# Kernel tuning notes

Hardware: AMD Instinct MI355X
Metric: run time of the kernel (lower is better)

The kernel has to match this reference:

```python
import jax, jax.numpy as jnp
import numpy as np

B, S, E, C, H = 64, 2048, 512, 512, 256


def setup_inputs() -> dict:
    key = jax.random.key(0)
    ks = jax.random.split(key, 8)
    encoder_word_embeds = jax.random.normal(ks[0], (B, S, E), dtype=jnp.float32)
    encoder_lengths = jax.random.randint(ks[1], (B,), 1, S + 1)  # lengths in [1, S]
    context_state = jax.random.normal(ks[2], (B, C), dtype=jnp.float32)
    # Learned parameters (nn.Linear style: y = x @ W.T + b)
    sw = 1.0 / np.sqrt(E)
    sc = 1.0 / np.sqrt(C)
    sh = 1.0 / np.sqrt(H)
    W_word = jax.random.uniform(ks[3], (H, E), minval=-sw, maxval=sw, dtype=jnp.float32)
    b_word = jax.random.uniform(ks[4], (H,), minval=-sw, maxval=sw, dtype=jnp.float32)
    W_ctx = jax.random.uniform(ks[5], (H, C), minval=-sc, maxval=sc, dtype=jnp.float32)
    b_ctx = jax.random.uniform(ks[6], (H,), minval=-sc, maxval=sc, dtype=jnp.float32)
    w_hidden = jax.random.uniform(ks[7], (H,), minval=-sh, maxval=sh, dtype=jnp.float32)  # hidden_layer has no bias
    return {
        "encoder_word_embeds": encoder_word_embeds,
        "encoder_lengths": encoder_lengths,
        "context_state": context_state,
        "W_word": W_word,
        "b_word": b_word,
        "W_ctx": W_ctx,
        "b_ctx": b_ctx,
        "w_hidden": w_hidden,
    }


def reference(encoder_word_embeds, encoder_lengths, context_state, W_word, b_word, W_ctx, b_ctx, w_hidden):
    seq_len = encoder_word_embeds.shape[1]
    # word mask [B, S]: positions < length
    positions = jnp.arange(seq_len)  # [S]
    mask = (positions[None, :] < encoder_lengths[:, None]).astype(jnp.float32)  # [B, S]
    # additive attention MLP
    word_feat = jnp.einsum("bse,he->bsh", encoder_word_embeds, W_word) + b_word  # [B,S,H]
    ctx_feat = context_state @ W_ctx.T + b_ctx  # [B,H]
    scores = jnp.einsum("bsh,h->bs", jnp.tanh(word_feat + ctx_feat[:, None, :]), w_hidden)  # [B,S]
    # softmax over seq, then mask and renormalize (matches original order)
    attn = jax.nn.softmax(scores, axis=1) * mask
    attn = attn / (1e-10 + attn.sum(axis=1, keepdims=True))  # [B,S]
    attention_features = jnp.einsum("bs,bse->be", attn, encoder_word_embeds)  # [B,E]
    return attention_features, attn
```

## Files before the change

### kernel.cpp

```cpp
#include <hip/hip_runtime.h>
#include <hip/hip_bf16.h>
#include <cstdint>
#include <cstddef>

#define B_  64
#define S_  2048
#define E_  512
#define C_  512
#define H_  256

using f32x4 = __attribute__((ext_vector_type(4))) float;
using s16x8 = __attribute__((ext_vector_type(8))) short;

__device__ __forceinline__ uint2 f4_to_bf4(float4 v) {
    __hip_bfloat162 lo = __float22bfloat162_rn(make_float2(v.x, v.y));
    __hip_bfloat162 hi = __float22bfloat162_rn(make_float2(v.z, v.w));
    union { __hip_bfloat162 b; unsigned u; } a, c;
    a.b = lo; c.b = hi;
    return make_uint2(a.u, c.u);
}

__device__ __forceinline__ void async16(const void* g, void* l) {
    __builtin_amdgcn_global_load_lds(
        (const __attribute__((address_space(1))) void*)g,
        (__attribute__((address_space(3))) void*)l,
        16, 0, 0);
}

__global__ void prep_kernel(const float* __restrict__ W, unsigned short* __restrict__ Wb,
                            const float* __restrict__ ctx, const float* __restrict__ Wc,
                            const float* __restrict__ bc, const float* __restrict__ bw,
                            float* __restrict__ cb) {
    __shared__ float row[C_];
    int blk = blockIdx.x, t = threadIdx.x;
    if (blk < 128) {
        int i = (blk * 256 + t) * 4;
        float4 v = *(const float4*)(W + i);
        *(uint2*)(Wb + i) = f4_to_bf4(v);
    } else {
        int b = blk - 128;
        row[t] = ctx[b * C_ + t];
        row[t + 256] = ctx[b * C_ + t + 256];
        __syncthreads();
        const float4* w4 = (const float4*)(Wc + (size_t)t * C_);
        const float4* x4 = (const float4*)row;
        float acc = 0.f;
        #pragma unroll 4
        for (int c = 0; c < C_ / 4; ++c) {
            float4 w = w4[c], x = x4[c];
            acc += w.x * x.x + w.y * x.y + w.z * x.z + w.w * x.w;
        }
        cb[b * H_ + t] = acc + bc[t] + bw[t];
    }
}

#define BM 128
#define BN 256
#define BK 64
#define LDT 72

__global__ __launch_bounds__(512) void scores_kernel(
    const float* __restrict__ A,
    const unsigned short* __restrict__ Wb,
    const float* __restrict__ cb,
    const float* __restrict__ wh,
    const int*   __restrict__ lens,
    float* __restrict__ scores)
{
    __shared__ __align__(16) unsigned short At[BM * LDT];
    __shared__ __align__(16) unsigned short Bt[BN * 64];
    __shared__ float sblk[BM];
    int t = threadIdx.x;
    int m0 = blockIdx.x * BM;
    int b  = m0 >> 11;
    int ms = m0 & (S_ - 1);
    if (ms >= lens[b]) return;

    int w = t >> 6, lane = t & 63, quad = lane >> 4, lm = lane & 15;
    int wm = (w & 1) * 64, wn = (w >> 1) * 64;

    if (t < BM) sblk[t] = 0.f;

    f32x4 acc[4][4] = {};

    int arow = t >> 4, acol = (t & 15) * 4;
    int la8 = lane >> 3, lc8 = lane & 7;

    for (int k0 = 0; k0 < E_; k0 += BK) {
        #pragma unroll
        for (int j = 0; j < 4; ++j) {
            int r  = (w << 5) + (j << 3) + la8;
            int cg = (lc8 ^ (r & 7)) << 3;
            async16(Wb + (size_t)r * E_ + k0 + cg,
                    (char*)Bt + (((w << 5) + (j << 3)) << 7));
        }
        #pragma unroll
        for (int i = 0; i < 4; ++i) {
            int r = arow + i * 32;
            float4 v = *(const float4*)(A + (size_t)(m0 + r) * E_ + k0 + acol);
            *(uint2*)(At + r * LDT + acol) = f4_to_bf4(v);
        }
        __syncthreads();
        #pragma unroll
        for (int ks = 0; ks < 2; ++ks) {
            s16x8 af[4], bfr[4];
            #pragma unroll
            for (int i = 0; i < 4; ++i)
                af[i] = *(const s16x8*)(At + (wm + i * 16 + lm) * LDT + ks * 32 + quad * 8);
            #pragma unroll
            for (int i = 0; i < 4; ++i) {
                int r = wn + i * 16 + lm;
                int c = (ks * 4 + quad) ^ (r & 7);
                bfr[i] = *(const s16x8*)(Bt + r * 64 + c * 8);
            }
            #pragma unroll
            for (int mi = 0; mi < 4; ++mi)
                #pragma unroll
                for (int ni = 0; ni < 4; ++ni)
                    acc[mi][ni] = __builtin_amdgcn_mfma_f32_16x16x32_bf16(
                        af[mi], bfr[ni], acc[mi][ni], 0, 0, 0);
        }
        __syncthreads();
    }

    float wv[4], cbv[4];
    #pragma unroll
    for (int ni = 0; ni < 4; ++ni) {
        int n = wn + ni * 16 + lm;
        wv[ni]  = wh[n];
        cbv[ni] = cb[b * H_ + n];
    }
    #pragma unroll
    for (int mi = 0; mi < 4; ++mi) {
        #pragma unroll
        for (int r = 0; r < 4; ++r) {
            float p = 0.f;
            #pragma unroll
            for (int ni = 0; ni < 4; ++ni) {
                float x = acc[mi][ni][r] + cbv[ni];
                x = fminf(fmaxf(x, -15.f), 15.f);
                float e = __expf(2.f * x);
                float th = 1.f - 2.f * __builtin_amdgcn_rcpf(e + 1.f);
                p += wv[ni] * th;
            }
            #pragma unroll
            for (int off = 8; off >= 1; off >>= 1)
                p += __shfl_xor(p, off);
            if (lm == 0)
                atomicAdd(&sblk[wm + mi * 16 + quad * 4 + r], p);
        }
    }
    __syncthreads();
    if (t < BM) scores[m0 + t] = sblk[t];
}

__global__ void softmax_kernel(const int* __restrict__ lens, float* __restrict__ attn,
                               float* __restrict__ feat) {
    __shared__ float redm[4], redt[4];
    int b = blockIdx.x, t = threadIdx.x;
    int len = lens[b];
    float* sc = attn + (size_t)b * S_;
    feat[b * E_ + t] = 0.f;
    feat[b * E_ + 256 + t] = 0.f;
    float v[8];
    #pragma unroll
    for (int i = 0; i < 8; ++i) {
        int s = t + i * 256;
        v[i] = (s < len) ? sc[s] : -1e30f;
    }
    float m = -1e30f;
    #pragma unroll
    for (int i = 0; i < 8; ++i) m = fmaxf(m, v[i]);
    #pragma unroll
    for (int off = 32; off >= 1; off >>= 1) m = fmaxf(m, __shfl_xor(m, off));
    if ((t & 63) == 0) redm[t >> 6] = m;
    __syncthreads();
    m = fmaxf(fmaxf(redm[0], redm[1]), fmaxf(redm[2], redm[3]));
    float e[8]; float tm = 0.f;
    #pragma unroll
    for (int i = 0; i < 8; ++i) {
        int s = t + i * 256;
        e[i] = (s < len) ? __expf(v[i] - m) : 0.f;
        tm += e[i];
    }
    #pragma unroll
    for (int off = 32; off >= 1; off >>= 1) tm += __shfl_xor(tm, off);
    if ((t & 63) == 0) redt[t >> 6] = tm;
    __syncthreads();
    tm = redt[0] + redt[1] + redt[2] + redt[3];
    float sfac = 1.f / tm;
    #pragma unroll
    for (int i = 0; i < 8; ++i) {
        int s = t + i * 256;
        sc[s] = e[i] * sfac;
    }
}

__global__ __launch_bounds__(512) void wsum_kernel(
    const float* __restrict__ A, const float* __restrict__ attn,
    const int* __restrict__ lens, float* __restrict__ out) {
    int b = blockIdx.y;
    int len = lens[b];
    int s0 = blockIdx.x * 128;
    if (s0 >= len) return;
    int send = s0 + 128; if (send > len) send = len;
    int t  = threadIdx.x;
    int e4 = t & 127;
    int sr = t >> 7;
    const float* ap = attn + (size_t)b * S_;
    f32x4 acc = {0.f, 0.f, 0.f, 0.f};
    const float* base = A + (size_t)b * S_ * E_;
    for (int s = s0 + sr; s < send; s += 4) {
        float wgt = ap[s];
        f32x4 v = *(const f32x4*)(base + (size_t)s * E_ + e4 * 4);
        acc += wgt * v;
    }
    __shared__ f32x4 red[4][128];
    red[sr][e4] = acc;
    __syncthreads();
    if (t < 128) {
        f32x4 tot = red[0][t] + red[1][t] + red[2][t] + red[3][t];
        float* o = out + (size_t)b * E_ + t * 4;
        atomicAdd(o + 0, tot[0]);
        atomicAdd(o + 1, tot[1]);
        atomicAdd(o + 2, tot[2]);
        atomicAdd(o + 3, tot[3]);
    }
}

extern "C" void kernel_launch(void* const* d_in, const int* in_sizes, int n_in,
                              void* d_out, int out_size, void* d_ws, size_t ws_size,
                              hipStream_t stream) {
    const float* embeds = (const float*)d_in[0];
    const int*   lens   = (const int*)d_in[1];
    const float* ctx    = (const float*)d_in[2];
    const float* Ww     = (const float*)d_in[3];
    const float* bw     = (const float*)d_in[4];
    const float* Wc     = (const float*)d_in[5];
    const float* bc     = (const float*)d_in[6];
    const float* wh     = (const float*)d_in[7];
    float* out  = (float*)d_out;
    float* feat = out;
    float* attn = out + B_ * E_;

    unsigned short* Wb = (unsigned short*)d_ws;
    float* cb = (float*)((char*)d_ws + (size_t)H_ * E_ * sizeof(unsigned short));

    prep_kernel<<<192, 256, 0, stream>>>(Ww, Wb, ctx, Wc, bc, bw, cb);
    scores_kernel<<<dim3(B_ * S_ / BM), 512, 0, stream>>>(embeds, Wb, cb, wh, lens, attn);
    softmax_kernel<<<B_, 256, 0, stream>>>(lens, attn, feat);
    wsum_kernel<<<dim3(S_ / 128, B_), 512, 0, stream>>>(embeds, attn, lens, feat);
}
```

Baseline: 407.4 us.

## Drop LDS staging in scores GEMM and load MFMA fragments directly from global

The scores kernel no longer stages A and W tiles in shared memory. Each wave now loads its bf16 W fragments and fp32 A rows straight from global memory into registers and converts A to bf16 in place. The block tile shrinks from 128 to 64 rows with 256 threads, and all four waves share the same A rows while splitting H. This removes the LDS traffic and the per-iteration barriers. In exchange, each A element is read from global (through the cache) by four waves, and the loads are uncoalesced 32-byte row segments with no software pipelining.

After: 522.4 us. +28.2%, slower.

```diff
diff --git a/kernel.cpp b/kernel.cpp
--- a/kernel.cpp
+++ b/kernel.cpp
@@ -20,11 +20,11 @@
     return make_uint2(a.u, c.u);
 }
 
-__device__ __forceinline__ void async16(const void* g, void* l) {
-    __builtin_amdgcn_global_load_lds(
-        (const __attribute__((address_space(1))) void*)g,
-        (__attribute__((address_space(3))) void*)l,
-        16, 0, 0);
+__device__ __forceinline__ s16x8 pack_bf8(float4 a, float4 b) {
+    union { s16x8 v; uint2 u[2]; } r;
+    r.u[0] = f4_to_bf4(a);
+    r.u[1] = f4_to_bf4(b);
+    return r.v;
 }
 
 __global__ void prep_kernel(const float* __restrict__ W, unsigned short* __restrict__ Wb,
@@ -54,12 +54,10 @@
     }
 }
 
-#define BM 128
-#define BN 256
+#define BM 64
 #define BK 64
-#define LDT 72
-
-__global__ __launch_bounds__(512) void scores_kernel(
+
+__global__ __launch_bounds__(256) void scores_kernel(
     const float* __restrict__ A,
     const unsigned short* __restrict__ Wb,
     const float* __restrict__ cb,
@@ -67,8 +65,6 @@
     const int*   __restrict__ lens,
     float* __restrict__ scores)
 {
-    __shared__ __align__(16) unsigned short At[BM * LDT];
-    __shared__ __align__(16) unsigned short Bt[BN * 64];
     __shared__ float sblk[BM];
     int t = threadIdx.x;
     int m0 = blockIdx.x * BM;
@@ -77,51 +73,43 @@
     if (ms >= lens[b]) return;
 
     int w = t >> 6, lane = t & 63, quad = lane >> 4, lm = lane & 15;
-    int wm = (w & 1) * 64, wn = (w >> 1) * 64;
+    int wn = w * 64;
 
     if (t < BM) sblk[t] = 0.f;
 
+    const float* a_base[4];
+    const unsigned short* b_base[4];
+    #pragma unroll
+    for (int i = 0; i < 4; ++i) {
+        a_base[i] = A  + (size_t)(m0 + i * 16 + lm) * E_ + quad * 8;
+        b_base[i] = Wb + (size_t)(wn + i * 16 + lm) * E_ + quad * 8;
+    }
+
     f32x4 acc[4][4] = {};
 
-    int arow = t >> 4, acol = (t & 15) * 4;
-    int la8 = lane >> 3, lc8 = lane & 7;
-
+    #pragma unroll 2
     for (int k0 = 0; k0 < E_; k0 += BK) {
         #pragma unroll
-        for (int j = 0; j < 4; ++j) {
-            int r  = (w << 5) + (j << 3) + la8;
-            int cg = (lc8 ^ (r & 7)) << 3;
-            async16(Wb + (size_t)r * E_ + k0 + cg,
-                    (char*)Bt + (((w << 5) + (j << 3)) << 7));
-        }
-        #pragma unroll
-        for (int i = 0; i < 4; ++i) {
-            int r = arow + i * 32;
-            float4 v = *(const float4*)(A + (size_t)(m0 + r) * E_ + k0 + acol);
-            *(uint2*)(At + r * LDT + acol) = f4_to_bf4(v);
-        }
-        __syncthreads();
-        #pragma unroll
         for (int ks = 0; ks < 2; ++ks) {
-            s16x8 af[4], bfr[4];
+            int ko = k0 + ks * 32;
+            s16x8 bfr[4];
             #pragma unroll
             for (int i = 0; i < 4; ++i)
-                af[i] = *(const s16x8*)(At + (wm + i * 16 + lm) * LDT + ks * 32 + quad * 8);
-            #pragma unroll
-            for (int i = 0; i < 4; ++i) {
-                int r = wn + i * 16 + lm;
-                int c = (ks * 4 + quad) ^ (r & 7);
-                bfr[i] = *(const s16x8*)(Bt + r * 64 + c * 8);
-            }
-            #pragma unroll
-            for (int mi = 0; mi < 4; ++mi)
+                bfr[i] = *(const s16x8*)(b_base[i] + ko);
+            #pragma unroll
+            for (int mi = 0; mi < 4; ++mi) {
+                const float* ap = a_base[mi] + ko;
+                float4 a0 = *(const float4*)ap;
+                float4 a1 = *(const float4*)(ap + 4);
+                s16x8 af = pack_bf8(a0, a1);
                 #pragma unroll
                 for (int ni = 0; ni < 4; ++ni)
                     acc[mi][ni] = __builtin_amdgcn_mfma_f32_16x16x32_bf16(
-                        af[mi], bfr[ni], acc[mi][ni], 0, 0, 0);
+                        af, bfr[ni], acc[mi][ni], 0, 0, 0);
+            }
         }
-        __syncthreads();
-    }
+    }
+    __syncthreads();
 
     float wv[4], cbv[4];
     #pragma unroll
@@ -147,7 +135,7 @@
             for (int off = 8; off >= 1; off >>= 1)
                 p += __shfl_xor(p, off);
             if (lm == 0)
-                atomicAdd(&sblk[wm + mi * 16 + quad * 4 + r], p);
+                atomicAdd(&sblk[mi * 16 + quad * 4 + r], p);
         }
     }
     __syncthreads();
@@ -247,7 +235,7 @@
     float* cb = (float*)((char*)d_ws + (size_t)H_ * E_ * sizeof(unsigned short));
 
     prep_kernel<<<192, 256, 0, stream>>>(Ww, Wb, ctx, Wc, bc, bw, cb);
-    scores_kernel<<<dim3(B_ * S_ / BM), 512, 0, stream>>>(embeds, Wb, cb, wh, lens, attn);
+    scores_kernel<<<dim3(B_ * S_ / BM), 256, 0, stream>>>(embeds, Wb, cb, wh, lens, attn);
     softmax_kernel<<<B_, 256, 0, stream>>>(lens, attn, feat);
     wsum_kernel<<<dim3(S_ / 128, B_), 512, 0, stream>>>(embeds, attn, lens, feat);
 }
```

## Fuse softmax and weighted sum into scores kernel via flash-style partials

Applied to the files above, without the earlier changes.

The scores kernel now computes a per-tile local max, exp-sum and exp-weighted sum of the embedding rows right after the scores, writing partial results to workspace. A small finalize kernel merges the partials with online-softmax rescaling, writes the features and normalizes the attention row. This removes the separate softmax and weighted-sum kernels and their second full read of the embeddings, which may now hit cache because the same tile was just loaded. In exchange the scores kernel gets a serial per-thread loop over 128 rows with strided fp32 loads, and the finalize step loops over partials serially.

Measured after the change: 418.9 us. +2.8%, slower.

```diff
diff --git a/kernel.cpp b/kernel.cpp
--- a/kernel.cpp
+++ b/kernel.cpp
@@ -65,16 +65,20 @@
     const float* __restrict__ cb,
     const float* __restrict__ wh,
     const int*   __restrict__ lens,
-    float* __restrict__ scores)
+    float* __restrict__ scores,
+    float* __restrict__ Wpart,
+    float* __restrict__ mtpart)
 {
     __shared__ __align__(16) unsigned short At[BM * LDT];
     __shared__ __align__(16) unsigned short Bt[BN * 64];
     __shared__ float sblk[BM];
+    __shared__ float pblk[BM];
     int t = threadIdx.x;
     int m0 = blockIdx.x * BM;
     int b  = m0 >> 11;
     int ms = m0 & (S_ - 1);
-    if (ms >= lens[b]) return;
+    int len = lens[b];
+    if (ms >= len) return;
 
     int w = t >> 6, lane = t & 63, quad = lane >> 4, lm = lane & 15;
     int wm = (w & 1) * 64, wn = (w >> 1) * 64;
@@ -152,79 +156,57 @@
     }
     __syncthreads();
     if (t < BM) scores[m0 + t] = sblk[t];
-}
-
-__global__ void softmax_kernel(const int* __restrict__ lens, float* __restrict__ attn,
-                               float* __restrict__ feat) {
-    __shared__ float redm[4], redt[4];
+
+    int nvalid = len - ms; if (nvalid > BM) nvalid = BM;
+    float m_l = -1e30f;
+    #pragma unroll 16
+    for (int r = 0; r < BM; ++r) {
+        float sv = (r < nvalid) ? sblk[r] : -1e30f;
+        m_l = fmaxf(m_l, sv);
+    }
+    if (t < BM) pblk[t] = (t < nvalid) ? __expf(sblk[t] - m_l) : 0.f;
+    __syncthreads();
+    float t_l = 0.f;
+    #pragma unroll 16
+    for (int r = 0; r < BM; ++r) t_l += pblk[r];
+    float accw = 0.f;
+    const float* ab = A + (size_t)m0 * E_ + t;
+    #pragma unroll 8
+    for (int r = 0; r < BM; ++r)
+        accw += pblk[r] * ab[(size_t)r * E_];
+    Wpart[(size_t)blockIdx.x * E_ + t] = accw;
+    if (t == 0) {
+        mtpart[blockIdx.x * 2 + 0] = m_l;
+        mtpart[blockIdx.x * 2 + 1] = t_l;
+    }
+}
+
+__global__ __launch_bounds__(512) void finalize_kernel(
+    const int* __restrict__ lens, const float* __restrict__ Wpart,
+    const float* __restrict__ mtpart,
+    float* __restrict__ attn,
+    float* __restrict__ feat)
+{
     int b = blockIdx.x, t = threadIdx.x;
     int len = lens[b];
+    int L = (len + BM - 1) / BM;
+    int base = b * (S_ / BM);
+    float M = -1e30f;
+    for (int l = 0; l < L; ++l) M = fmaxf(M, mtpart[(base + l) * 2]);
+    float T = 0.f;
+    for (int l = 0; l < L; ++l)
+        T += __expf(mtpart[(base + l) * 2] - M) * mtpart[(base + l) * 2 + 1];
+    float inv = 1.f / T;
+    float acc = 0.f;
+    for (int l = 0; l < L; ++l)
+        acc += __expf(mtpart[(base + l) * 2] - M) * Wpart[(size_t)(base + l) * E_ + t];
+    feat[b * E_ + t] = acc * inv;
     float* sc = attn + (size_t)b * S_;
-    feat[b * E_ + t] = 0.f;
-    feat[b * E_ + 256 + t] = 0.f;
-    float v[8];
     #pragma unroll
-    for (int i = 0; i < 8; ++i) {
-        int s = t + i * 256;
-        v[i] = (s < len) ? sc[s] : -1e30f;
-    }
-    float m = -1e30f;
-    #pragma unroll
-    for (int i = 0; i < 8; ++i) m = fmaxf(m, v[i]);
-    #pragma unroll
-    for (int off = 32; off >= 1; off >>= 1) m = fmaxf(m, __shfl_xor(m, off));
-    if ((t & 63) == 0) redm[t >> 6] = m;
-    __syncthreads();
-    m = fmaxf(fmaxf(redm[0], redm[1]), fmaxf(redm[2], redm[3]));
-    float e[8]; float tm = 0.f;
-    #pragma unroll
-    for (int i = 0; i < 8; ++i) {
-        int s = t + i * 256;
-        e[i] = (s < len) ? __expf(v[i] - m) : 0.f;
-        tm += e[i];
-    }
-    #pragma unroll
-    for (int off = 32; off >= 1; off >>= 1) tm += __shfl_xor(tm, off);
-    if ((t & 63) == 0) redt[t >> 6] = tm;
-    __syncthreads();
-    tm = redt[0] + redt[1] + redt[2] + redt[3];
-    float sfac = 1.f / tm;
-    #pragma unroll
-    for (int i = 0; i < 8; ++i) {
-        int s = t + i * 256;
-        sc[s] = e[i] * sfac;
-    }
-}
-
-__global__ __launch_bounds__(512) void wsum_kernel(
-    const float* __restrict__ A, const float* __restrict__ attn,
-    const int* __restrict__ lens, float* __restrict__ out) {
-    int b = blockIdx.y;
-    int len = lens[b];
-    int s0 = blockIdx.x * 128;
-    if (s0 >= len) return;
-    int send = s0 + 128; if (send > len) send = len;
-    int t  = threadIdx.x;
-    int e4 = t & 127;
-    int sr = t >> 7;
-    const float* ap = attn + (size_t)b * S_;
-    f32x4 acc = {0.f, 0.f, 0.f, 0.f};
-    const float* base = A + (size_t)b * S_ * E_;
-    for (int s = s0 + sr; s < send; s += 4) {
-        float wgt = ap[s];
-        f32x4 v = *(const f32x4*)(base + (size_t)s * E_ + e4 * 4);
-        acc += wgt * v;
-    }
-    __shared__ f32x4 red[4][128];
-    red[sr][e4] = acc;
-    __syncthreads();
-    if (t < 128) {
-        f32x4 tot = red[0][t] + red[1][t] + red[2][t] + red[3][t];
-        float* o = out + (size_t)b * E_ + t * 4;
-        atomicAdd(o + 0, tot[0]);
-        atomicAdd(o + 1, tot[1]);
-        atomicAdd(o + 2, tot[2]);
-        atomicAdd(o + 3, tot[3]);
+    for (int i = 0; i < 4; ++i) {
+        int s = t + i * 512;
+        float v = sc[s];
+        sc[s] = (s < len) ? __expf(v - M) * inv : 0.f;
     }
 }
 
@@ -243,11 +225,14 @@
     float* feat = out;
     float* attn = out + B_ * E_;
 
-    unsigned short* Wb = (unsigned short*)d_ws;
-    float* cb = (float*)((char*)d_ws + (size_t)H_ * E_ * sizeof(unsigned short));
+    char* ws = (char*)d_ws;
+    unsigned short* Wb = (unsigned short*)ws;
+    float* cb     = (float*)(ws + 256 * 1024);
+    float* Wpart  = (float*)(ws + 320 * 1024);
+    float* mtpart = (float*)(ws + 320 * 1024 + 2 * 1024 * 1024);
 
     prep_kernel<<<192, 256, 0, stream>>>(Ww, Wb, ctx, Wc, bc, bw, cb);
-    scores_kernel<<<dim3(B_ * S_ / BM), 512, 0, stream>>>(embeds, Wb, cb, wh, lens, attn);
-    softmax_kernel<<<B_, 256, 0, stream>>>(lens, attn, feat);
-    wsum_kernel<<<dim3(S_ / 128, B_), 512, 0, stream>>>(embeds, attn, lens, feat);
-}
+    scores_kernel<<<dim3(B_ * S_ / BM), 512, 0, stream>>>(embeds, Wb, cb, wh, lens,
+                                                          attn, Wpart, mtpart);
+    finalize_kernel<<<B_, 512, 0, stream>>>(lens, Wpart, mtpart, attn, feat);
+}
```

## Double-buffer scores GEMM tiles with prefetch and smaller K step

Applied to the files above, without the earlier changes.

The scores GEMM now keeps two LDS buffers for both the bf16 A tile and the async-loaded weight tile. The next K slice's global loads are issued before the MFMAs on the current slice, so memory latency overlaps with compute, and there is one barrier per step instead of two. BK drops from 64 to 32 with a matching XOR swizzle and padding, and the launch bounds now request 4 blocks per CU. The cost is twice as many loop iterations, more register pressure from the prefetched values, and a tighter register budget that could spill.

New measurement: 410.9 us. No clear change (+0.9%).

```diff
diff --git a/kernel.cpp b/kernel.cpp
--- a/kernel.cpp
+++ b/kernel.cpp
@@ -18,6 +18,13 @@
     union { __hip_bfloat162 b; unsigned u; } a, c;
     a.b = lo; c.b = hi;
     return make_uint2(a.u, c.u);
+}
+
+__device__ __forceinline__ s16x8 pack_bf8(float4 a, float4 b) {
+    union { s16x8 v; uint2 u[2]; } r;
+    r.u[0] = f4_to_bf4(a);
+    r.u[1] = f4_to_bf4(b);
+    return r.v;
 }
 
 __device__ __forceinline__ void async16(const void* g, void* l) {
@@ -56,10 +63,11 @@
 
 #define BM 128
 #define BN 256
-#define BK 64
-#define LDT 72
-
-__global__ __launch_bounds__(512) void scores_kernel(
+#define BK 32
+#define NT (E_ / BK)
+#define LDT 40
+
+__global__ __launch_bounds__(512, 4) void scores_kernel(
     const float* __restrict__ A,
     const unsigned short* __restrict__ Wb,
     const float* __restrict__ cb,
@@ -67,8 +75,8 @@
     const int*   __restrict__ lens,
     float* __restrict__ scores)
 {
-    __shared__ __align__(16) unsigned short At[BM * LDT];
-    __shared__ __align__(16) unsigned short Bt[BN * 64];
+    __shared__ __align__(16) unsigned short At[2][BM * LDT];
+    __shared__ __align__(16) unsigned short Bt[2][BN * BK];
     __shared__ float sblk[BM];
     int t = threadIdx.x;
     int m0 = blockIdx.x * BM;
@@ -83,35 +91,49 @@
 
     f32x4 acc[4][4] = {};
 
-    int arow = t >> 4, acol = (t & 15) * 4;
-    int la8 = lane >> 3, lc8 = lane & 7;
-
-    for (int k0 = 0; k0 < E_; k0 += BK) {
-        #pragma unroll
-        for (int j = 0; j < 4; ++j) {
-            int r  = (w << 5) + (j << 3) + la8;
-            int cg = (lc8 ^ (r & 7)) << 3;
-            async16(Wb + (size_t)r * E_ + k0 + cg,
-                    (char*)Bt + (((w << 5) + (j << 3)) << 7));
-        }
-        #pragma unroll
-        for (int i = 0; i < 4; ++i) {
-            int r = arow + i * 32;
-            float4 v = *(const float4*)(A + (size_t)(m0 + r) * E_ + k0 + acol);
-            *(uint2*)(At + r * LDT + acol) = f4_to_bf4(v);
-        }
-        __syncthreads();
-        #pragma unroll
-        for (int ks = 0; ks < 2; ++ks) {
+    int arow = t >> 2, acol = (t & 3) * 8;
+    const float* asrc = A + (size_t)(m0 + arow) * E_ + acol;
+    unsigned short* adst0 = At[0] + arow * LDT + acol;
+    unsigned short* adst1 = At[1] + arow * LDT + acol;
+
+    int rb = (w << 5) + (lane >> 2);
+    int cb4 = lane & 3;
+    const unsigned short* bs0 = Wb + (size_t)rb * E_ + ((cb4 ^ (rb & 3)) << 3);
+    const unsigned short* bs1 = bs0 + (size_t)16 * E_;
+    int bofs0 = w << 11;
+    int bofs1 = bofs0 + 1024;
+
+    {
+        async16(bs0, (char*)Bt[0] + bofs0);
+        async16(bs1, (char*)Bt[0] + bofs1);
+        float4 a0 = *(const float4*)(asrc);
+        float4 a1 = *(const float4*)(asrc + 4);
+        *(s16x8*)adst0 = pack_bf8(a0, a1);
+    }
+    __syncthreads();
+
+    int cur = 0;
+    for (int step = 0; step < NT; ++step) {
+        bool pf = (step < NT - 1);
+        int k1 = (step + 1) * BK;
+        float4 av0, av1;
+        if (pf) {
+            av0 = *(const float4*)(asrc + k1);
+            av1 = *(const float4*)(asrc + k1 + 4);
+            async16(bs0 + k1, (char*)Bt[cur ^ 1] + bofs0);
+            async16(bs1 + k1, (char*)Bt[cur ^ 1] + bofs1);
+        }
+        {
+            const unsigned short* Atc = At[cur];
+            const unsigned short* Btc = Bt[cur];
             s16x8 af[4], bfr[4];
             #pragma unroll
             for (int i = 0; i < 4; ++i)
-                af[i] = *(const s16x8*)(At + (wm + i * 16 + lm) * LDT + ks * 32 + quad * 8);
+                af[i] = *(const s16x8*)(Atc + (wm + i * 16 + lm) * LDT + quad * 8);
             #pragma unroll
             for (int i = 0; i < 4; ++i) {
                 int r = wn + i * 16 + lm;
-                int c = (ks * 4 + quad) ^ (r & 7);
-                bfr[i] = *(const s16x8*)(Bt + r * 64 + c * 8);
+                bfr[i] = *(const s16x8*)(Btc + r * BK + ((quad ^ (r & 3)) << 3));
             }
             #pragma unroll
             for (int mi = 0; mi < 4; ++mi)
@@ -120,7 +142,12 @@
                     acc[mi][ni] = __builtin_amdgcn_mfma_f32_16x16x32_bf16(
                         af[mi], bfr[ni], acc[mi][ni], 0, 0, 0);
         }
-        __syncthreads();
+        if (pf) {
+            *(s16x8*)(cur ? adst0 : adst1) = pack_bf8(av0, av1);
+        }
+        asm volatile("s_waitcnt vmcnt(0) lgkmcnt(0)" ::: "memory");
+        __builtin_amdgcn_s_barrier();
+        cur ^= 1;
     }
 
     float wv[4], cbv[4];
```
